# Kernel tuning notes

Hardware: AMD Instinct MI355X
Metric: run time of the kernel (lower is better)

The kernel has to match this reference:

```python
import jax, jax.numpy as jnp
import numpy as np

N_ENTITIES = 100000
EMBED_DIM = 128
N_EDGES = 1600000
LEAKY_SLOPE = 0.01  # nn.LeakyReLU default


def setup_inputs() -> dict:
    key = jax.random.key(0)
    k1, k2, k3, k4, k5, k6, k7, k8 = jax.random.split(key, 8)
    entity_embs = jax.random.normal(k1, (N_ENTITIES, EMBED_DIM), dtype=jnp.float32)
    adj_rows = jax.random.randint(k2, (N_EDGES,), 0, N_ENTITIES, dtype=jnp.int32)
    adj_cols = jax.random.randint(k3, (N_EDGES,), 0, N_ENTITIES, dtype=jnp.int32)
    adj_vals = jax.random.uniform(k4, (N_EDGES,), dtype=jnp.float32)
    s = 1.0 / np.sqrt(EMBED_DIM)  # nn.Linear default init scale
    W_self = jax.random.uniform(k5, (EMBED_DIM, EMBED_DIM), jnp.float32, -s, s)
    b_self = jax.random.uniform(k6, (EMBED_DIM,), jnp.float32, -s, s)
    W_neigh = jax.random.uniform(k7, (EMBED_DIM, EMBED_DIM), jnp.float32, -s, s)
    b_neigh = jax.random.uniform(k8, (EMBED_DIM,), jnp.float32, -s, s)
    return {"entity_embs": entity_embs, "adj_rows": adj_rows, "adj_cols": adj_cols,
            "adj_vals": adj_vals, "W_self": W_self, "b_self": b_self,
            "W_neigh": W_neigh, "b_neigh": b_neigh}


def reference(entity_embs, adj_rows, adj_cols, adj_vals, W_self, b_self, W_neigh, b_neigh):
    # self path: Linear(input_dim, output_dim) -> x @ W.T + b
    self_emb = entity_embs @ W_self.T + b_self  # [N, D]
    # neighbor path: sparse adjacency SpMM (COO): out[r] += v * embs[c]
    contrib = adj_vals[:, None] * entity_embs[adj_cols]  # [E, D]
    neigh = jax.ops.segment_sum(contrib, adj_rows, num_segments=N_ENTITIES)  # [N, D]
    neigh_emb = neigh @ W_neigh.T + b_neigh
    out = jax.nn.leaky_relu(self_emb + neigh_emb, negative_slope=LEAKY_SLOPE)
    # dropout is identity in eval mode
    return out
```

## Files before the change

### kernel.cpp

```cpp
#include <hip/hip_runtime.h>

#define DIM 128
#define TILE_R 32
#define CAP 64

typedef __attribute__((ext_vector_type(8))) short short8;
typedef __attribute__((ext_vector_type(4))) float floatx4;

static __device__ __forceinline__ short f2bf(float x) {
    unsigned u = __float_as_uint(x);
    u = (u + 0x7FFF + ((u >> 16) & 1)) >> 16;
    return (short)u;
}
static __device__ __forceinline__ float bflo(unsigned p) { return __uint_as_float(p << 16); }
static __device__ __forceinline__ float bfhi(unsigned p) { return __uint_as_float(p & 0xFFFF0000u); }

__global__ __launch_bounds__(256) void zero_kernel(float4* __restrict__ out, int n4) {
    int i = blockIdx.x * 256 + threadIdx.x;
    if (i < n4) out[i] = make_float4(0.f, 0.f, 0.f, 0.f);
}

__global__ __launch_bounds__(256) void zero_counts_kernel(int* __restrict__ cnt,
                                                          int* __restrict__ cursor, int n) {
    int i = blockIdx.x * 256 + threadIdx.x;
    if (i < n) cnt[i] = 0;
    if (i == 0) *cursor = 0;
}

__global__ __launch_bounds__(256) void initA_kernel(int* __restrict__ next, int n) {
    int i = blockIdx.x * 256 + threadIdx.x;
    if (i < n) next[i] = i * CAP;
}

__global__ __launch_bounds__(256) void hist_kernel(const int* __restrict__ rows,
                                                   int* __restrict__ cnt, int nE) {
    int i4 = (blockIdx.x * 256 + threadIdx.x) * 4;
    if (i4 + 3 < nE) {
        int4 r = *(const int4*)(rows + i4);
        atomicAdd(&cnt[r.x], 1);
        atomicAdd(&cnt[r.y], 1);
        atomicAdd(&cnt[r.z], 1);
        atomicAdd(&cnt[r.w], 1);
    } else {
        for (int k = 0; k < 4 && i4 + k < nE; k++) atomicAdd(&cnt[rows[i4 + k]], 1);
    }
}

__global__ __launch_bounds__(256) void offsets_kernel(int* __restrict__ next,
                                                      int* __restrict__ start,
                                                      int* __restrict__ cursor, int n) {
    int i = blockIdx.x * 256 + threadIdx.x;
    int lane = threadIdx.x & 63;
    int c = (i < n) ? next[i] : 0;
    int s = c;
#pragma unroll
    for (int d = 1; d < 64; d <<= 1) {
        int t = __shfl_up(s, d);
        if (lane >= d) s += t;
    }
    int total = __shfl(s, 63);
    int base = 0;
    if (lane == 63) base = atomicAdd(cursor, total);
    base = __shfl(base, 63);
    int off = base + s - c;
    if (i < n) {
        start[i] = off;
        next[i] = off;
    }
}

template <bool CAPPED>
__global__ __launch_bounds__(256) void fill_kernel(const int* __restrict__ rows,
                                                   const int* __restrict__ cols,
                                                   const float* __restrict__ vals,
                                                   int* __restrict__ next,
                                                   int2* __restrict__ csr, int nE) {
    int i4 = (blockIdx.x * 256 + threadIdx.x) * 4;
    if (i4 + 3 < nE) {
        int4 r = *(const int4*)(rows + i4);
        int4 c = *(const int4*)(cols + i4);
        float4 v = *(const float4*)(vals + i4);
        int p0 = atomicAdd(&next[r.x], 1);
        int p1 = atomicAdd(&next[r.y], 1);
        int p2 = atomicAdd(&next[r.z], 1);
        int p3 = atomicAdd(&next[r.w], 1);
        if (!CAPPED || p0 < r.x * CAP + CAP) csr[p0] = make_int2(c.x, __float_as_int(v.x));
        if (!CAPPED || p1 < r.y * CAP + CAP) csr[p1] = make_int2(c.y, __float_as_int(v.y));
        if (!CAPPED || p2 < r.z * CAP + CAP) csr[p2] = make_int2(c.z, __float_as_int(v.z));
        if (!CAPPED || p3 < r.w * CAP + CAP) csr[p3] = make_int2(c.w, __float_as_int(v.w));
    } else {
        for (int k = 0; k < 4 && i4 + k < nE; k++) {
            int rr = rows[i4 + k];
            int p = atomicAdd(&next[rr], 1);
            if (!CAPPED || p < rr * CAP + CAP)
                csr[p] = make_int2(cols[i4 + k], __float_as_int(vals[i4 + k]));
        }
    }
}

__global__ __launch_bounds__(256) void wprep_kernel(const float* __restrict__ Wself,
                                                    const float* __restrict__ Wneigh,
                                                    short* __restrict__ Wf) {
    int idx = blockIdx.x * 256 + threadIdx.x;
    int t = idx >> 8;
    int s = (idx >> 6) & 3;
    int lane = idx & 63;
    int n = (t & 7) * 16 + (lane & 15);
    int k0 = s * 32 + (lane >> 4) * 8;
    const float* row = (t < 8 ? Wself : Wneigh) + (size_t)n * DIM + k0;
    short8 v;
#pragma unroll
    for (int j = 0; j < 8; j++) v[j] = f2bf(row[j]);
    *(short8*)(Wf + (size_t)idx * 8) = v;
}

__global__ __launch_bounds__(256) void gemm_kernel(const float* __restrict__ embs,
                                                   const short* __restrict__ Wf,
                                                   unsigned short* __restrict__ Sb,
                                                   unsigned short* __restrict__ Yb,
                                                   int nRows) {
    int wave = threadIdx.x >> 6;
    int lane = threadIdx.x & 63;
    int quad = lane >> 4;
    int m0 = blockIdx.x * 64 + wave * 16;
    int m = m0 + (lane & 15);
    bool valid = m < nRows;

    const float* Arow = embs + (size_t)m * DIM;
    short8 a[4];
#pragma unroll
    for (int s = 0; s < 4; s++) {
        float4 f0 = make_float4(0.f, 0.f, 0.f, 0.f), f1 = f0;
        if (valid) {
            f0 = *(const float4*)(Arow + s * 32 + quad * 8);
            f1 = *(const float4*)(Arow + s * 32 + quad * 8 + 4);
        }
        short8 av;
        av[0] = f2bf(f0.x); av[1] = f2bf(f0.y); av[2] = f2bf(f0.z); av[3] = f2bf(f0.w);
        av[4] = f2bf(f1.x); av[5] = f2bf(f1.y); av[6] = f2bf(f1.z); av[7] = f2bf(f1.w);
        a[s] = av;
    }

    const short8* WfV = (const short8*)Wf;
#pragma unroll
    for (int t = 0; t < 16; t++) {
        floatx4 acc = {0.f, 0.f, 0.f, 0.f};
#pragma unroll
        for (int s = 0; s < 4; s++) {
            short8 b = WfV[(t * 4 + s) * 64 + lane];
            acc = __builtin_amdgcn_mfma_f32_16x16x32_bf16(a[s], b, acc, 0, 0, 0);
        }
        int col = t * 16 + (lane & 15);
        unsigned short* dst = (col < DIM) ? (Sb + col) : (Yb + (col - DIM));
#pragma unroll
        for (int reg = 0; reg < 4; reg++) {
            int grow = m0 + quad * 4 + reg;
            if (grow < nRows) dst[(size_t)grow * DIM] = (unsigned short)f2bf(acc[reg]);
        }
    }
}

template <bool CAPPED>
__global__ __launch_bounds__(256) void gatherY_kernel(const unsigned* __restrict__ Sb,
                                                      const unsigned* __restrict__ Yb,
                                                      const int* __restrict__ start,
                                                      const int* __restrict__ next,
                                                      const int2* __restrict__ csr,
                                                      const float* __restrict__ bself,
                                                      const float* __restrict__ bneigh,
                                                      float* __restrict__ out, int nRows) {
    int r = blockIdx.x * 4 + (threadIdx.x >> 6);
    if (r >= nRows) return;
    int lane = threadIdx.x & 63;
    int s, e;
    if (CAPPED) {
        s = r * CAP;
        e = min(__builtin_amdgcn_readfirstlane(next[r]), s + CAP);
    } else {
        s = __builtin_amdgcn_readfirstlane(start[r]);
        e = __builtin_amdgcn_readfirstlane(next[r]);
    }
    float ax = 0.f, ay = 0.f;
    int j = s;
    for (; j + 4 <= e; j += 4) {
        int2 c0 = csr[j], c1 = csr[j + 1], c2 = csr[j + 2], c3 = csr[j + 3];
        unsigned y0 = Yb[(size_t)c0.x * 64 + lane];
        unsigned y1 = Yb[(size_t)c1.x * 64 + lane];
        unsigned y2 = Yb[(size_t)c2.x * 64 + lane];
        unsigned y3 = Yb[(size_t)c3.x * 64 + lane];
        float v0 = __int_as_float(c0.y), v1 = __int_as_float(c1.y);
        float v2 = __int_as_float(c2.y), v3 = __int_as_float(c3.y);
        ax += v0 * bflo(y0) + v1 * bflo(y1) + v2 * bflo(y2) + v3 * bflo(y3);
        ay += v0 * bfhi(y0) + v1 * bfhi(y1) + v2 * bfhi(y2) + v3 * bfhi(y3);
    }
    for (; j < e; j++) {
        int2 c = csr[j];
        float v = __int_as_float(c.y);
        unsigned y = Yb[(size_t)c.x * 64 + lane];
        ax += v * bflo(y);
        ay += v * bfhi(y);
    }
    unsigned sp = __builtin_nontemporal_load(&Sb[(size_t)r * 64 + lane]);
    float ox = bflo(sp) + bself[2 * lane] + bneigh[2 * lane] + ax;
    float oy = bfhi(sp) + bself[2 * lane + 1] + bneigh[2 * lane + 1] + ay;
    ox = ox > 0.f ? ox : 0.01f * ox;
    oy = oy > 0.f ? oy : 0.01f * oy;
    union { float2 f; double d; } u;
    u.f = make_float2(ox, oy);
    __builtin_nontemporal_store(u.d, (double*)(out + (size_t)r * DIM + lane * 2));
}

__global__ __launch_bounds__(256) void gather_embs_kernel(const float2* __restrict__ embs2,
                                                          const int* __restrict__ start,
                                                          const int* __restrict__ next,
                                                          const int2* __restrict__ csr,
                                                          float* __restrict__ out, int nRows) {
    int r = blockIdx.x * 4 + (threadIdx.x >> 6);
    if (r >= nRows) return;
    int lane = threadIdx.x & 63;
    int s = start[r];
    int e = next[r];
    float2 acc = make_float2(0.f, 0.f);
    for (int b = s; b < e; b += 64) {
        int n = min(64, e - b);
        int2 cv = make_int2(0, 0);
        if (lane < n) cv = csr[b + lane];
        float vf = __int_as_float(cv.y);
        for (int j = 0; j < n; j++) {
            int cj = __shfl(cv.x, j);
            float vj = __shfl(vf, j);
            float2 x = embs2[(size_t)cj * 64 + lane];
            acc.x += vj * x.x;
            acc.y += vj * x.y;
        }
    }
    ((float2*)out)[(size_t)r * 64 + lane] = acc;
}

__global__ __launch_bounds__(256) void scatter_kernel(
    const float* __restrict__ embs, const int* __restrict__ rows,
    const int* __restrict__ cols, const float* __restrict__ vals,
    float* __restrict__ out, int nE) {
    int e = blockIdx.x * 4 + (threadIdx.x >> 6);
    if (e >= nE) return;
    int lane = threadIdx.x & 63;
    int r = rows[e];
    int c = cols[e];
    float v = vals[e];
    float2 x = ((const float2*)(embs + (size_t)c * DIM))[lane];
    float* dst = out + (size_t)r * DIM + lane * 2;
    unsafeAtomicAdd(dst, v * x.x);
    unsafeAtomicAdd(dst + 1, v * x.y);
}

__global__ __launch_bounds__(256) void fused_kernel(
    const float* __restrict__ embs, const float* __restrict__ Wself,
    const float* __restrict__ bself, const float* __restrict__ Wneigh,
    const float* __restrict__ bneigh, float* __restrict__ out, int nRows) {
    __shared__ float xs[TILE_R][DIM];
    __shared__ float xn[TILE_R][DIM];

    int r0 = blockIdx.x * TILE_R;
    if (r0 >= nRows) return;

    const float4* gs = (const float4*)(embs + (size_t)r0 * DIM);
    const float4* gn = (const float4*)(out + (size_t)r0 * DIM);
    float4* sxs = (float4*)&xs[0][0];
    float4* sxn = (float4*)&xn[0][0];
    for (int i = threadIdx.x; i < TILE_R * DIM / 4; i += 256) {
        sxs[i] = gs[i];
        sxn[i] = gn[i];
    }
    __syncthreads();

    int j = threadIdx.x & 127;
    int rbase = (threadIdx.x >> 7) * 16;

    const float4* ws = (const float4*)(Wself + (size_t)j * DIM);
    const float4* wn = (const float4*)(Wneigh + (size_t)j * DIM);

    float acc[16];
#pragma unroll
    for (int i = 0; i < 16; i++) acc[i] = 0.f;

    for (int k4 = 0; k4 < DIM / 4; k4++) {
        float4 a = ws[k4];
        float4 b = wn[k4];
#pragma unroll
        for (int rr = 0; rr < 16; rr++) {
            float4 x = *(const float4*)&xs[rbase + rr][k4 * 4];
            float4 y = *(const float4*)&xn[rbase + rr][k4 * 4];
            acc[rr] += x.x * a.x + x.y * a.y + x.z * a.z + x.w * a.w
                     + y.x * b.x + y.y * b.y + y.z * b.z + y.w * b.w;
        }
    }

    float bias = bself[j] + bneigh[j];
#pragma unroll
    for (int rr = 0; rr < 16; rr++) {
        float v = acc[rr] + bias;
        out[(size_t)(r0 + rbase + rr) * DIM + j] = v > 0.f ? v : 0.01f * v;
    }
}

static inline size_t a16(size_t x) { return (x + 15) & ~(size_t)15; }

extern "C" void kernel_launch(void* const* d_in, const int* in_sizes, int n_in,
                              void* d_out, int out_size, void* d_ws, size_t ws_size,
                              hipStream_t stream) {
    const float* embs   = (const float*)d_in[0];
    const int*   rows   = (const int*)d_in[1];
    const int*   cols   = (const int*)d_in[2];
    const float* vals   = (const float*)d_in[3];
    const float* Wself  = (const float*)d_in[4];
    const float* bself  = (const float*)d_in[5];
    const float* Wneigh = (const float*)d_in[6];
    const float* bneigh = (const float*)d_in[7];
    float* out = (float*)d_out;

    int nE = in_sizes[1];
    int nRows = out_size / DIM;
    size_t wfBytes = (size_t)16 * 4 * 64 * 8 * 2;
    size_t bfPlane = (size_t)nRows * DIM * 2;

    size_t A_next = 0;
    size_t A_buck = A_next + a16((size_t)nRows * 4);
    size_t A_wf   = A_buck + a16((size_t)nRows * CAP * 8);
    size_t A_y    = A_wf + a16(wfBytes);
    size_t A_s    = A_y + bfPlane;
    size_t needA  = A_s + bfPlane;

    size_t B_next  = 0;
    size_t B_start = B_next + a16((size_t)nRows * 4);
    size_t B_cur   = B_start + a16((size_t)nRows * 4);
    size_t B_csr   = B_cur + 16;
    size_t B_wf    = B_csr + a16((size_t)nE * 8);
    size_t B_y     = B_wf + a16(wfBytes);
    size_t B_s     = B_y + bfPlane;
    size_t needB   = B_s + bfPlane;

    size_t C_csr  = a16((size_t)(2 * nRows + 1) * 4);
    size_t needC  = C_csr + (size_t)nE * 8;

    int rb = (nRows + 255) / 256;
    int eb4 = (nE / 4 + 255) / 256;

    if (ws_size >= needA) {
        int*  next = (int*)((char*)d_ws + A_next);
        int2* csr  = (int2*)((char*)d_ws + A_buck);
        short* Wf  = (short*)((char*)d_ws + A_wf);
        unsigned short* Yb = (unsigned short*)((char*)d_ws + A_y);
        unsigned short* Sb = (unsigned short*)((char*)d_ws + A_s);

        initA_kernel<<<rb, 256, 0, stream>>>(next, nRows);
        fill_kernel<true><<<eb4, 256, 0, stream>>>(rows, cols, vals, next, csr, nE);
        wprep_kernel<<<16, 256, 0, stream>>>(Wself, Wneigh, Wf);
        gemm_kernel<<<(nRows + 63) / 64, 256, 0, stream>>>(embs, Wf, Sb, Yb, nRows);
        gatherY_kernel<true><<<(nRows + 3) / 4, 256, 0, stream>>>(
            (const unsigned*)Sb, (const unsigned*)Yb, nullptr, next, csr,
            bself, bneigh, out, nRows);
    } else if (ws_size >= needB) {
        int*  next   = (int*)((char*)d_ws + B_next);
        int*  start  = (int*)((char*)d_ws + B_start);
        int*  cursor = (int*)((char*)d_ws + B_cur);
        int2* csr    = (int2*)((char*)d_ws + B_csr);
        short* Wf    = (short*)((char*)d_ws + B_wf);
        unsigned short* Yb = (unsigned short*)((char*)d_ws + B_y);
        unsigned short* Sb = (unsigned short*)((char*)d_ws + B_s);

        zero_counts_kernel<<<rb, 256, 0, stream>>>(next, cursor, nRows);
        hist_kernel<<<eb4, 256, 0, stream>>>(rows, next, nE);
        offsets_kernel<<<rb, 256, 0, stream>>>(next, start, cursor, nRows);
        fill_kernel<false><<<eb4, 256, 0, stream>>>(rows, cols, vals, next, csr, nE);
        wprep_kernel<<<16, 256, 0, stream>>>(Wself, Wneigh, Wf);
        gemm_kernel<<<(nRows + 63) / 64, 256, 0, stream>>>(embs, Wf, Sb, Yb, nRows);
        gatherY_kernel<false><<<(nRows + 3) / 4, 256, 0, stream>>>(
            (const unsigned*)Sb, (const unsigned*)Yb, start, next, csr,
            bself, bneigh, out, nRows);
    } else if (ws_size >= needC) {
        int* next = (int*)d_ws;
        int* start = next + nRows;
        int* cursor = start + nRows;
        int2* csr = (int2*)((char*)d_ws + C_csr);

        zero_counts_kernel<<<rb, 256, 0, stream>>>(next, cursor, nRows);
        hist_kernel<<<eb4, 256, 0, stream>>>(rows, next, nE);
        offsets_kernel<<<rb, 256, 0, stream>>>(next, start, cursor, nRows);
        fill_kernel<false><<<eb4, 256, 0, stream>>>(rows, cols, vals, next, csr, nE);
        gather_embs_kernel<<<(nRows + 3) / 4, 256, 0, stream>>>(
            (const float2*)embs, start, next, csr, out, nRows);
        fused_kernel<<<(nRows + TILE_R - 1) / TILE_R, 256, 0, stream>>>(
            embs, Wself, bself, Wneigh, bneigh, out, nRows);
    } else {
        int n4 = out_size / 4;
        zero_kernel<<<(n4 + 255) / 256, 256, 0, stream>>>((float4*)out, n4);
        scatter_kernel<<<(nE + 3) / 4, 256, 0, stream>>>(embs, rows, cols, vals, out, nE);
        fused_kernel<<<(nRows + TILE_R - 1) / TILE_R, 256, 0, stream>>>(
            embs, Wself, bself, Wneigh, bneigh, out, nRows);
    }
}
```

Before: 363.7 us.

## Region-partition bucket fill by row range and store edge indices instead of pairs

Path A now merges the weight conversion and bucket init into one prep kernel. Bucket filling becomes a kernel in which blocks are assigned to row regions (8 regions x 128 edge chunks), so the atomics and scattered writes of a block stay in one row range, aiming for cache or XCD locality. Each block writes only a 4-byte edge index instead of a col/val pair. The gather then loads cols and vals indirectly through that index, which adds a dependent random load per edge in exchange for cheaper fill writes and less bucket memory. Every block also reads the full rows array once per region, so rows is read eight times in total.

```diff
diff --git a/kernel.cpp b/kernel.cpp
--- a/kernel.cpp
+++ b/kernel.cpp
@@ -3,6 +3,8 @@
 #define DIM 128
 #define TILE_R 32
 #define CAP 64
+#define NREG 8
+#define NCHUNK 128
 
 typedef __attribute__((ext_vector_type(8))) short short8;
 typedef __attribute__((ext_vector_type(4))) float floatx4;
@@ -27,9 +29,60 @@
     if (i == 0) *cursor = 0;
 }
 
-__global__ __launch_bounds__(256) void initA_kernel(int* __restrict__ next, int n) {
-    int i = blockIdx.x * 256 + threadIdx.x;
-    if (i < n) next[i] = i * CAP;
+__global__ __launch_bounds__(256) void prep_kernel(const float* __restrict__ Wself,
+                                                   const float* __restrict__ Wneigh,
+                                                   short* __restrict__ Wf,
+                                                   int* __restrict__ next, int nRows) {
+    int idx = blockIdx.x * 256 + threadIdx.x;
+    if (idx < 4096) {
+        int t = idx >> 8;
+        int s = (idx >> 6) & 3;
+        int lane = idx & 63;
+        int n = (t & 7) * 16 + (lane & 15);
+        int k0 = s * 32 + (lane >> 4) * 8;
+        const float* row = (t < 8 ? Wself : Wneigh) + (size_t)n * DIM + k0;
+        short8 v;
+#pragma unroll
+        for (int j = 0; j < 8; j++) v[j] = f2bf(row[j]);
+        *(short8*)(Wf + (size_t)idx * 8) = v;
+    }
+    int r = idx - 4096;
+    if (r >= 0 && r < nRows) next[r] = r * CAP;
+}
+
+__global__ __launch_bounds__(256) void fill_xcd_kernel(const int* __restrict__ rows,
+                                                       int* __restrict__ next,
+                                                       int* __restrict__ perm,
+                                                       int nE, int nRows) {
+    int region = blockIdx.x & (NREG - 1);
+    int chunk = blockIdx.x / NREG;
+    int rowsPerReg = (nRows + NREG - 1) / NREG;
+    int rowLo = region * rowsPerReg;
+    int rowHi = min(rowLo + rowsPerReg, nRows);
+    int per = (nE + NCHUNK - 1) / NCHUNK;
+    per = (per + 3) & ~3;
+    int s = chunk * per;
+    int e = min(s + per, nE);
+
+    for (int base = s + threadIdx.x * 4; base < e; base += 256 * 4) {
+        int r4[4];
+        int cnt = 4;
+        if (base + 3 < e) {
+            int4 v = *(const int4*)(rows + base);
+            r4[0] = v.x; r4[1] = v.y; r4[2] = v.z; r4[3] = v.w;
+        } else {
+            cnt = e - base;
+            for (int k = 0; k < cnt; k++) r4[k] = rows[base + k];
+        }
+#pragma unroll 4
+        for (int k = 0; k < cnt; k++) {
+            int rr = r4[k];
+            if (rr >= rowLo && rr < rowHi) {
+                int p = atomicAdd(&next[rr], 1);
+                if (p < rr * CAP + CAP) perm[p] = base + k;
+            }
+        }
+    }
 }
 
 __global__ __launch_bounds__(256) void hist_kernel(const int* __restrict__ rows,
@@ -69,12 +122,11 @@
     }
 }
 
-template <bool CAPPED>
-__global__ __launch_bounds__(256) void fill_kernel(const int* __restrict__ rows,
-                                                   const int* __restrict__ cols,
-                                                   const float* __restrict__ vals,
-                                                   int* __restrict__ next,
-                                                   int2* __restrict__ csr, int nE) {
+__global__ __launch_bounds__(256) void fillB_kernel(const int* __restrict__ rows,
+                                                    const int* __restrict__ cols,
+                                                    const float* __restrict__ vals,
+                                                    int* __restrict__ next,
+                                                    int2* __restrict__ csr, int nE) {
     int i4 = (blockIdx.x * 256 + threadIdx.x) * 4;
     if (i4 + 3 < nE) {
         int4 r = *(const int4*)(rows + i4);
@@ -84,16 +136,14 @@
         int p1 = atomicAdd(&next[r.y], 1);
         int p2 = atomicAdd(&next[r.z], 1);
         int p3 = atomicAdd(&next[r.w], 1);
-        if (!CAPPED || p0 < r.x * CAP + CAP) csr[p0] = make_int2(c.x, __float_as_int(v.x));
-        if (!CAPPED || p1 < r.y * CAP + CAP) csr[p1] = make_int2(c.y, __float_as_int(v.y));
-        if (!CAPPED || p2 < r.z * CAP + CAP) csr[p2] = make_int2(c.z, __float_as_int(v.z));
-        if (!CAPPED || p3 < r.w * CAP + CAP) csr[p3] = make_int2(c.w, __float_as_int(v.w));
+        csr[p0] = make_int2(c.x, __float_as_int(v.x));
+        csr[p1] = make_int2(c.y, __float_as_int(v.y));
+        csr[p2] = make_int2(c.z, __float_as_int(v.z));
+        csr[p3] = make_int2(c.w, __float_as_int(v.w));
     } else {
         for (int k = 0; k < 4 && i4 + k < nE; k++) {
-            int rr = rows[i4 + k];
-            int p = atomicAdd(&next[rr], 1);
-            if (!CAPPED || p < rr * CAP + CAP)
-                csr[p] = make_int2(cols[i4 + k], __float_as_int(vals[i4 + k]));
+            int p = atomicAdd(&next[rows[i4 + k]], 1);
+            csr[p] = make_int2(cols[i4 + k], __float_as_int(vals[i4 + k]));
         }
     }
 }
@@ -160,7 +210,50 @@
     }
 }
 
-template <bool CAPPED>
+__global__ __launch_bounds__(256) void gatherY_perm_kernel(const unsigned* __restrict__ Sb,
+                                                           const unsigned* __restrict__ Yb,
+                                                           const int* __restrict__ next,
+                                                           const int* __restrict__ perm,
+                                                           const int* __restrict__ cols,
+                                                           const float* __restrict__ vals,
+                                                           const float* __restrict__ bself,
+                                                           const float* __restrict__ bneigh,
+                                                           float* __restrict__ out, int nRows) {
+    int r = blockIdx.x * 4 + (threadIdx.x >> 6);
+    if (r >= nRows) return;
+    int lane = threadIdx.x & 63;
+    int s = r * CAP;
+    int e = min(__builtin_amdgcn_readfirstlane(next[r]), s + CAP);
+    float ax = 0.f, ay = 0.f;
+    int j = s;
+    for (; j + 4 <= e; j += 4) {
+        int4 p4 = *(const int4*)(perm + j);
+        int c0 = cols[p4.x], c1 = cols[p4.y], c2 = cols[p4.z], c3 = cols[p4.w];
+        float v0 = vals[p4.x], v1 = vals[p4.y], v2 = vals[p4.z], v3 = vals[p4.w];
+        unsigned y0 = Yb[(size_t)c0 * 64 + lane];
+        unsigned y1 = Yb[(size_t)c1 * 64 + lane];
+        unsigned y2 = Yb[(size_t)c2 * 64 + lane];
+        unsigned y3 = Yb[(size_t)c3 * 64 + lane];
+        ax += v0 * bflo(y0) + v1 * bflo(y1) + v2 * bflo(y2) + v3 * bflo(y3);
+        ay += v0 * bfhi(y0) + v1 * bfhi(y1) + v2 * bfhi(y2) + v3 * bfhi(y3);
+    }
+    for (; j < e; j++) {
+        int p = perm[j];
+        float v = vals[p];
+        unsigned y = Yb[(size_t)cols[p] * 64 + lane];
+        ax += v * bflo(y);
+        ay += v * bfhi(y);
+    }
+    unsigned sp = __builtin_nontemporal_load(&Sb[(size_t)r * 64 + lane]);
+    float ox = bflo(sp) + bself[2 * lane] + bneigh[2 * lane] + ax;
+    float oy = bfhi(sp) + bself[2 * lane + 1] + bneigh[2 * lane + 1] + ay;
+    ox = ox > 0.f ? ox : 0.01f * ox;
+    oy = oy > 0.f ? oy : 0.01f * oy;
+    union { float2 f; double d; } u;
+    u.f = make_float2(ox, oy);
+    __builtin_nontemporal_store(u.d, (double*)(out + (size_t)r * DIM + lane * 2));
+}
+
 __global__ __launch_bounds__(256) void gatherY_kernel(const unsigned* __restrict__ Sb,
                                                       const unsigned* __restrict__ Yb,
                                                       const int* __restrict__ start,
@@ -172,14 +265,8 @@
     int r = blockIdx.x * 4 + (threadIdx.x >> 6);
     if (r >= nRows) return;
     int lane = threadIdx.x & 63;
-    int s, e;
-    if (CAPPED) {
-        s = r * CAP;
-        e = min(__builtin_amdgcn_readfirstlane(next[r]), s + CAP);
-    } else {
-        s = __builtin_amdgcn_readfirstlane(start[r]);
-        e = __builtin_amdgcn_readfirstlane(next[r]);
-    }
+    int s = __builtin_amdgcn_readfirstlane(start[r]);
+    int e = __builtin_amdgcn_readfirstlane(next[r]);
     float ax = 0.f, ay = 0.f;
     int j = s;
     for (; j + 4 <= e; j += 4) {
@@ -325,7 +412,7 @@
 
     size_t A_next = 0;
     size_t A_buck = A_next + a16((size_t)nRows * 4);
-    size_t A_wf   = A_buck + a16((size_t)nRows * CAP * 8);
+    size_t A_wf   = A_buck + a16((size_t)nRows * CAP * 4);
     size_t A_y    = A_wf + a16(wfBytes);
     size_t A_s    = A_y + bfPlane;
     size_t needA  = A_s + bfPlane;
@@ -347,17 +434,16 @@
 
     if (ws_size >= needA) {
         int*  next = (int*)((char*)d_ws + A_next);
-        int2* csr  = (int2*)((char*)d_ws + A_buck);
+        int*  perm = (int*)((char*)d_ws + A_buck);
         short* Wf  = (short*)((char*)d_ws + A_wf);
         unsigned short* Yb = (unsigned short*)((char*)d_ws + A_y);
         unsigned short* Sb = (unsigned short*)((char*)d_ws + A_s);
 
-        initA_kernel<<<rb, 256, 0, stream>>>(next, nRows);
-        fill_kernel<true><<<eb4, 256, 0, stream>>>(rows, cols, vals, next, csr, nE);
-        wprep_kernel<<<16, 256, 0, stream>>>(Wself, Wneigh, Wf);
+        prep_kernel<<<(4096 + nRows + 255) / 256, 256, 0, stream>>>(Wself, Wneigh, Wf, next, nRows);
+        fill_xcd_kernel<<<NREG * NCHUNK, 256, 0, stream>>>(rows, next, perm, nE, nRows);
         gemm_kernel<<<(nRows + 63) / 64, 256, 0, stream>>>(embs, Wf, Sb, Yb, nRows);
-        gatherY_kernel<true><<<(nRows + 3) / 4, 256, 0, stream>>>(
-            (const unsigned*)Sb, (const unsigned*)Yb, nullptr, next, csr,
+        gatherY_perm_kernel<<<(nRows + 3) / 4, 256, 0, stream>>>(
+            (const unsigned*)Sb, (const unsigned*)Yb, next, perm, cols, vals,
             bself, bneigh, out, nRows);
     } else if (ws_size >= needB) {
         int*  next   = (int*)((char*)d_ws + B_next);
@@ -371,10 +457,10 @@
         zero_counts_kernel<<<rb, 256, 0, stream>>>(next, cursor, nRows);
         hist_kernel<<<eb4, 256, 0, stream>>>(rows, next, nE);
         offsets_kernel<<<rb, 256, 0, stream>>>(next, start, cursor, nRows);
-        fill_kernel<false><<<eb4, 256, 0, stream>>>(rows, cols, vals, next, csr, nE);
+        fillB_kernel<<<eb4, 256, 0, stream>>>(rows, cols, vals, next, csr, nE);
         wprep_kernel<<<16, 256, 0, stream>>>(Wself, Wneigh, Wf);
         gemm_kernel<<<(nRows + 63) / 64, 256, 0, stream>>>(embs, Wf, Sb, Yb, nRows);
-        gatherY_kernel<false><<<(nRows + 3) / 4, 256, 0, stream>>>(
+        gatherY_kernel<<<(nRows + 3) / 4, 256, 0, stream>>>(
             (const unsigned*)Sb, (const unsigned*)Yb, start, next, csr,
             bself, bneigh, out, nRows);
     } else if (ws_size >= needC) {
@@ -386,7 +472,7 @@
         zero_counts_kernel<<<rb, 256, 0, stream>>>(next, cursor, nRows);
         hist_kernel<<<eb4, 256, 0, stream>>>(rows, next, nE);
         offsets_kernel<<<rb, 256, 0, stream>>>(next, start, cursor, nRows);
-        fill_kernel<false><<<eb4, 256, 0, stream>>>(rows, cols, vals, next, csr, nE);
+        fillB_kernel<<<eb4, 256, 0, stream>>>(rows, cols, vals, next, csr, nE);
         gather_embs_kernel<<<(nRows + 3) / 4, 256, 0, stream>>>(
             (const float2*)embs, start, next, csr, out, nRows);
         fused_kernel<<<(nRows + TILE_R - 1) / TILE_R, 256, 0, stream>>>(
```

Result: faster. 332.0 us (-8.7%).
